# Kernel tuning notes

Hardware: AMD Instinct MI355X
Metric: run time of the kernel (lower is better)

Reference implementation:

```python
import jax, jax.numpy as jnp
import numpy as np

MAX_DIST = 10
N_OUT = 8


def setup_inputs() -> dict:
    key = jax.random.key(0)
    k1, k2 = jax.random.split(key)
    B, N = 32, 512
    adjacency = jax.random.uniform(k1, (B, N, N), dtype=jnp.float32)
    node_mask = jnp.ones((B, N), dtype=bool)
    # learned embedding table: (max_distance + 2, n_out)
    emb = jax.random.normal(k2, (MAX_DIST + 2, N_OUT), dtype=jnp.float32)
    return {"adjacency": adjacency, "node_mask": node_mask, "emb": emb}


def reference(adjacency, node_mask, emb):
    # BFS distances computed under no_grad in the original -> stop_gradient
    adjacency = jax.lax.stop_gradient(adjacency)
    B, N, _ = adjacency.shape
    adj_bin = adjacency > 0.5
    adj_sym = adj_bin | jnp.swapaxes(adj_bin, -1, -2)
    pair_valid = node_mask[:, :, None] & node_mask[:, None, :]  # (B,N,N)
    adj_sym = adj_sym & pair_valid
    adj_f = adj_sym.astype(jnp.float32)

    UNREACH = MAX_DIST + 1
    eye = jnp.eye(N, dtype=bool)[None]                 # (1,N,N)
    dist = jnp.where(eye, 0, UNREACH).astype(jnp.int32)  # broadcasts to (B,N,N) later
    reach = jnp.broadcast_to(eye, (B, N, N))

    # iterative BFS: reach_{k+1} = (reach_k @ adj > 0) | reach_k
    for k in range(1, MAX_DIST + 1):
        reach_next = (jnp.einsum('bij,bjk->bik', reach.astype(jnp.float32), adj_f) > 0) | reach
        frontier = reach_next & ~reach
        dist = jnp.where(frontier, jnp.int32(k), dist)
        reach = reach_next

    dist = jnp.where(pair_valid, dist, UNREACH)  # invalid pairs -> UNREACHABLE
    return emb[dist]  # (B,N,N,n_out)
```

## Files before the change

### kernel.cpp

```cpp
#include <hip/hip_runtime.h>
#include <stdint.h>

typedef unsigned long long u64;
typedef float vf4 __attribute__((ext_vector_type(4)));

#define NB 32
#define N 512
#define MAXD 10
#define NW 8
#define ST 516
#define PB 8

__global__ __launch_bounds__(256) void k1_pack(const float* __restrict__ adj,
                                               const int* __restrict__ mask,
                                               u64* __restrict__ gsym) {
    __shared__ u64 pa[64];
    __shared__ u64 pb[64];
    __shared__ u64 mwIJ[2];
    int p = blockIdx.x;
    int b = blockIdx.y;
    int ti = 0;
    while (p >= 8 - ti) { p -= 8 - ti; ++ti; }
    int tj = ti + p;
    int i0 = ti * 64, j0 = tj * 64;
    int t = threadIdx.x, wave = t >> 6, lane = t & 63;
    const float* Ab = adj + (size_t)b * N * N;
    #pragma unroll 4
    for (int s = 0; s < 16; ++s) {
        int r = wave * 16 + s;
        bool ba = Ab[(size_t)(i0 + r) * N + j0 + lane] > 0.5f;
        u64 wa = __ballot(ba);
        bool bb = Ab[(size_t)(j0 + r) * N + i0 + lane] > 0.5f;
        u64 wb = __ballot(bb);
        if (lane == 0) { pa[r] = wa; pb[r] = wb; }
    }
    if (wave < 2) {
        u64 m = __ballot(mask[b * N + (wave == 0 ? i0 : j0) + lane] != 0);
        if (lane == 0) mwIJ[wave] = m;
    }
    __syncthreads();

    if (wave < 2) {
        u64 x = (wave == 0) ? pb[lane] : pa[lane];
        const u64 Hm[6] = {0xFFFFFFFF00000000ULL, 0xFFFF0000FFFF0000ULL,
                           0xFF00FF00FF00FF00ULL, 0xF0F0F0F0F0F0F0F0ULL,
                           0xCCCCCCCCCCCCCCCCULL, 0xAAAAAAAAAAAAAAAAULL};
        #pragma unroll
        for (int k = 0; k < 6; ++k) {
            int j = 32 >> k;
            u64 H = Hm[k];
            u64 y = (u64)__shfl_xor((unsigned long long)x, j);
            x = ((lane & j) == 0) ? ((x & ~H) | ((y << j) & H))
                                  : ((x & H) | ((y >> j) & ~H));
        }
        u64 own  = (wave == 0) ? pa[lane] : pb[lane];
        u64 mrow = mwIJ[wave];
        u64 mcol = mwIJ[wave ^ 1];
        u64 outw = (own | x) & (((mrow >> lane) & 1) ? mcol : 0ULL);
        size_t row = (size_t)b * N + (wave == 0 ? i0 : j0) + lane;
        int wt = (wave == 0) ? tj : ti;
        gsym[row * NW + wt] = outw;
    }
}

__device__ __forceinline__ u64 spread8(unsigned b) {
    u64 x = (u64)(b * 0x01010101u);
    x |= x << 32;
    x &= 0x8040201008040201ULL;
    x += 0x7f7f7f7f7f7f7f7fULL;
    return (x >> 7) & 0x0101010101010101ULL;
}

__global__ __launch_bounds__(256) void k2_bfs(const u64* __restrict__ gsym,
                                              const int* __restrict__ mask,
                                              u64* __restrict__ distw) {
    __shared__ u64 adjT[NW * ST];
    __shared__ u64 outB[64 * 65];
    int blk = blockIdx.x;
    int b = blk >> 3;
    int r0 = (blk & 7) * 64;
    int t = threadIdx.x;
    const u64* gs = gsym + (size_t)b * N * NW;
    for (int q = t; q < N * NW; q += 256) {
        u64 w = gs[q];
        adjT[(q & 7) * ST + (q >> 3)] = w;
    }
    __syncthreads();

    if (t < 64) {
        int i = r0 + t;
        bool mi = mask[b * N + i] != 0;
        u64 c0[NW], c1[NW], c2[NW], c3[NW];
        #pragma unroll
        for (int w = 0; w < NW; ++w) { c0[w] = 0; c1[w] = 0; c2[w] = 0; c3[w] = 0; }

        if (mi) {
            u64 reach[NW] = {};
            u64 frontier[NW] = {};
            reach[i >> 6] = 1ULL << (i & 63);
            #pragma unroll
            for (int w = 0; w < NW; ++w) frontier[w] = reach[w];
            bool active = true;
            for (int k = 0; k <= MAXD; ++k) {
                u64 nr_any = 0;
                #pragma unroll
                for (int w = 0; w < NW; ++w) {
                    u64 u = ~reach[w];
                    nr_any |= u;
                    u64 t0 = c0[w] & u; c0[w] ^= u;
                    u64 t1 = c1[w] & t0; c1[w] ^= t0;
                    u64 t2 = c2[w] & t1; c2[w] ^= t1;
                    c3[w] ^= t2;
                }
                if (nr_any == 0) break;
                if (k == MAXD) break;
                if (active) {
                    u64 acc[NW] = {};
                    bool sat = false;
                    for (int w = 0; w < NW && !sat; ++w) {
                        u64 f = frontier[w];
                        while (f && !sat) {
                            int jlast = w << 6;
                            #pragma unroll
                            for (int u = 0; u < PB; ++u) {
                                int j = f ? ((w << 6) + __builtin_ctzll(f)) : jlast;
                                jlast = j;
                                f &= f - 1;
                                #pragma unroll
                                for (int e = 0; e < NW; ++e) acc[e] |= adjT[e * ST + j];
                            }
                            u64 all = acc[0];
                            #pragma unroll
                            for (int e = 1; e < NW; ++e) all &= acc[e];
                            sat = (all == ~0ULL);
                        }
                    }
                    bool any = false;
                    #pragma unroll
                    for (int w = 0; w < NW; ++w) {
                        u64 nf = acc[w] & ~reach[w];
                        frontier[w] = nf;
                        reach[w] |= nf;
                        any = any || (nf != 0);
                    }
                    active = any;
                }
            }
        } else {
            #pragma unroll
            for (int w = 0; w < NW; ++w) { c0[w] = ~0ULL; c1[w] = ~0ULL; c3[w] = ~0ULL; }
        }

        #pragma unroll
        for (int w = 0; w < NW; ++w) {
            #pragma unroll
            for (int h = 0; h < 8; ++h) {
                unsigned b0 = (unsigned)(c0[w] >> (8 * h)) & 0xFF;
                unsigned b1 = (unsigned)(c1[w] >> (8 * h)) & 0xFF;
                unsigned b2 = (unsigned)(c2[w] >> (8 * h)) & 0xFF;
                unsigned b3 = (unsigned)(c3[w] >> (8 * h)) & 0xFF;
                outB[t * 65 + w * 8 + h] =
                    spread8(b0) | (spread8(b1) << 1) | (spread8(b2) << 2) | (spread8(b3) << 3);
            }
        }
    }
    __syncthreads();

    u64* dp = distw + ((size_t)(b * N + r0)) * 64;
    for (int q = t; q < 64 * 64; q += 256) {
        dp[q] = outB[(q >> 6) * 65 + (q & 63)];
    }
}

__global__ __launch_bounds__(256) void k3_expand(const u64* __restrict__ distw,
                                                 const float* __restrict__ emb,
                                                 vf4* __restrict__ out4) {
    __shared__ vf4 e4[(MAXD + 2) * 2];
    int t = threadIdx.x;
    if (t < (MAXD + 2) * 2) e4[t] = ((const vf4*)emb)[t];
    __syncthreads();
    const unsigned char* __restrict__ db = (const unsigned char*)distw;
    size_t dbase = (size_t)blockIdx.x * 4096;
    const unsigned char* dp = db + dbase;
    vf4* op = out4 + dbase * 2;
    int h = t & 1;
    int tb = t >> 1;
    #pragma unroll 8
    for (int g = 0; g < 16; ++g) {
        int d0 = dp[g * 256 + tb];
        int d1 = dp[g * 256 + 128 + tb];
        vf4 v0 = e4[d0 * 2 + h];
        vf4 v1 = e4[d1 * 2 + h];
        op[g * 512 + t] = v0;
        op[g * 512 + 256 + t] = v1;
    }
}

extern "C" void kernel_launch(void* const* d_in, const int* in_sizes, int n_in,
                              void* d_out, int out_size, void* d_ws, size_t ws_size,
                              hipStream_t stream) {
    const float* adj = (const float*)d_in[0];
    const int* mask = (const int*)d_in[1];
    const float* emb = (const float*)d_in[2];
    u64* distw = (u64*)d_ws;
    u64* gsym = (u64*)((char*)d_ws + (size_t)NB * N * N);
    k1_pack<<<dim3(36, NB), 256, 0, stream>>>(adj, mask, gsym);
    k2_bfs<<<dim3(NB * 8), 256, 0, stream>>>(gsym, mask, distw);
    k3_expand<<<dim3(2048), 256, 0, stream>>>(distw, emb, (vf4*)d_out);
}
```

Before: 318.1 us.

## Spread BFS over more blocks with fewer sources each, parallelize distance expansion

The BFS kernel now handles 16 source rows per block instead of 64 and launches four times as many blocks (1024), so more CUs run the serial per-thread BFS at the same time. The first BFS step copies the source's adjacency row directly instead of going through the frontier loop. The bit-sliced distance counters are written raw to shared memory, and the spread-to-byte conversion runs across all 256 threads instead of 64. In exchange, each block reloads the whole 32 KB packed adjacency for fewer sources, which adds redundant global and LDS traffic, and only 16 threads per block do the BFS work.

```diff
diff --git a/kernel.cpp b/kernel.cpp
--- a/kernel.cpp
+++ b/kernel.cpp
@@ -10,6 +10,7 @@
 #define NW 8
 #define ST 516
 #define PB 8
+#define SRC 16
 
 __global__ __launch_bounds__(256) void k1_pack(const float* __restrict__ adj,
                                                const int* __restrict__ mask,
@@ -75,19 +76,18 @@
                                               const int* __restrict__ mask,
                                               u64* __restrict__ distw) {
     __shared__ u64 adjT[NW * ST];
-    __shared__ u64 outB[64 * 65];
+    __shared__ u64 cd[SRC][NW][4];
     int blk = blockIdx.x;
-    int b = blk >> 3;
-    int r0 = (blk & 7) * 64;
+    int b = blk >> 5;
+    int r0 = (blk & 31) * SRC;
     int t = threadIdx.x;
     const u64* gs = gsym + (size_t)b * N * NW;
     for (int q = t; q < N * NW; q += 256) {
-        u64 w = gs[q];
-        adjT[(q & 7) * ST + (q >> 3)] = w;
-    }
-    __syncthreads();
-
-    if (t < 64) {
+        adjT[(q & 7) * ST + (q >> 3)] = gs[q];
+    }
+    __syncthreads();
+
+    if (t < SRC) {
         int i = r0 + t;
         bool mi = mask[b * N + i] != 0;
         u64 c0[NW], c1[NW], c2[NW], c3[NW];
@@ -98,8 +98,6 @@
             u64 reach[NW] = {};
             u64 frontier[NW] = {};
             reach[i >> 6] = 1ULL << (i & 63);
-            #pragma unroll
-            for (int w = 0; w < NW; ++w) frontier[w] = reach[w];
             bool active = true;
             for (int k = 0; k <= MAXD; ++k) {
                 u64 nr_any = 0;
@@ -115,24 +113,31 @@
                 if (nr_any == 0) break;
                 if (k == MAXD) break;
                 if (active) {
-                    u64 acc[NW] = {};
+                    u64 acc[NW];
                     bool sat = false;
-                    for (int w = 0; w < NW && !sat; ++w) {
-                        u64 f = frontier[w];
-                        while (f && !sat) {
-                            int jlast = w << 6;
-                            #pragma unroll
-                            for (int u = 0; u < PB; ++u) {
-                                int j = f ? ((w << 6) + __builtin_ctzll(f)) : jlast;
-                                jlast = j;
-                                f &= f - 1;
+                    if (k == 0) {
+                        #pragma unroll
+                        for (int e = 0; e < NW; ++e) acc[e] = adjT[e * ST + i];
+                    } else {
+                        #pragma unroll
+                        for (int e = 0; e < NW; ++e) acc[e] = 0;
+                        for (int w = 0; w < NW && !sat; ++w) {
+                            u64 f = frontier[w];
+                            while (f && !sat) {
+                                int jlast = w << 6;
                                 #pragma unroll
-                                for (int e = 0; e < NW; ++e) acc[e] |= adjT[e * ST + j];
+                                for (int u = 0; u < PB; ++u) {
+                                    int j = f ? ((w << 6) + __builtin_ctzll(f)) : jlast;
+                                    jlast = j;
+                                    f &= f - 1;
+                                    #pragma unroll
+                                    for (int e = 0; e < NW; ++e) acc[e] |= adjT[e * ST + j];
+                                }
+                                u64 all = acc[0];
+                                #pragma unroll
+                                for (int e = 1; e < NW; ++e) all &= acc[e];
+                                sat = (all == ~0ULL);
                             }
-                            u64 all = acc[0];
-                            #pragma unroll
-                            for (int e = 1; e < NW; ++e) all &= acc[e];
-                            sat = (all == ~0ULL);
                         }
                     }
                     bool any = false;
@@ -153,22 +158,26 @@
 
         #pragma unroll
         for (int w = 0; w < NW; ++w) {
-            #pragma unroll
-            for (int h = 0; h < 8; ++h) {
-                unsigned b0 = (unsigned)(c0[w] >> (8 * h)) & 0xFF;
-                unsigned b1 = (unsigned)(c1[w] >> (8 * h)) & 0xFF;
-                unsigned b2 = (unsigned)(c2[w] >> (8 * h)) & 0xFF;
-                unsigned b3 = (unsigned)(c3[w] >> (8 * h)) & 0xFF;
-                outB[t * 65 + w * 8 + h] =
-                    spread8(b0) | (spread8(b1) << 1) | (spread8(b2) << 2) | (spread8(b3) << 3);
-            }
+            cd[t][w][0] = c0[w];
+            cd[t][w][1] = c1[w];
+            cd[t][w][2] = c2[w];
+            cd[t][w][3] = c3[w];
         }
     }
     __syncthreads();
 
+    const unsigned char* cb = (const unsigned char*)cd;
     u64* dp = distw + ((size_t)(b * N + r0)) * 64;
-    for (int q = t; q < 64 * 64; q += 256) {
-        dp[q] = outB[(q >> 6) * 65 + (q & 63)];
+    #pragma unroll
+    for (int g = 0; g < (SRC * 64) / 256; ++g) {
+        int q = t + 256 * g;
+        int s = q >> 6, v = q & 63, w = v >> 3, h = v & 7;
+        int base = ((s * NW + w) * 4) * 8 + h;
+        unsigned b0 = cb[base];
+        unsigned b1 = cb[base + 8];
+        unsigned b2 = cb[base + 16];
+        unsigned b3 = cb[base + 24];
+        dp[q] = spread8(b0) | (spread8(b1) << 1) | (spread8(b2) << 2) | (spread8(b3) << 3);
     }
 }
 
@@ -205,6 +214,6 @@
     u64* distw = (u64*)d_ws;
     u64* gsym = (u64*)((char*)d_ws + (size_t)NB * N * N);
     k1_pack<<<dim3(36, NB), 256, 0, stream>>>(adj, mask, gsym);
-    k2_bfs<<<dim3(NB * 8), 256, 0, stream>>>(gsym, mask, distw);
+    k2_bfs<<<dim3(NB * 32), 256, 0, stream>>>(gsym, mask, distw);
     k3_expand<<<dim3(2048), 256, 0, stream>>>(distw, emb, (vf4*)d_out);
 }
```

After: 321.6 us. Within noise of the previous version (+1.1%).
